# Kernel optimization log

Measured on AMD Instinct MI355X. Metric: run time of the kernel, lower is better.

## Reference

```python
import jax, jax.numpy as jnp
import numpy as np

NUM_EMBEDDINGS = 8192
EMBEDDING_DIM = 512
COMMITMENT_COST = 0.25
DECAY = 0.99
EPSILON = 1e-05


def setup_inputs() -> dict:
    key = jax.random.key(0)
    k1, k2, k3, k4 = jax.random.split(key, 4)
    z = jax.random.normal(k1, (16, 2048, EMBEDDING_DIM), dtype=jnp.float32)
    weight = jax.random.normal(k2, (NUM_EMBEDDINGS, EMBEDDING_DIM), dtype=jnp.float32)
    ema_cluster_size = jax.random.uniform(k3, (NUM_EMBEDDINGS,), dtype=jnp.float32)
    ema_w = jax.random.normal(k4, (NUM_EMBEDDINGS, EMBEDDING_DIM), dtype=jnp.float32)
    return {"z": z, "weight": weight, "ema_cluster_size": ema_cluster_size, "ema_w": ema_w}


def reference(z, weight, ema_cluster_size, ema_w):
    K, D = weight.shape
    z_flat = z.reshape(-1, D)                                   # [N, D]
    # squared-distance matrix via expanded GEMM (same math as torch)
    dist = ((z_flat ** 2).sum(1, keepdims=True)
            + (weight ** 2).sum(1)
            - 2.0 * z_flat @ weight.T)                          # [N, K]
    codes = jnp.argmin(dist, axis=1)                            # [N]
    # training-mode EMA update: one-hot sums expressed as segment_sum
    counts = jax.ops.segment_sum(jnp.ones(z_flat.shape[0], dtype=z.dtype), codes, num_segments=K)
    dw = jax.ops.segment_sum(z_flat, codes, num_segments=K)     # encodings.T @ z_flat
    new_cs = ema_cluster_size * DECAY + (1.0 - DECAY) * counts
    new_ema_w = ema_w * DECAY + (1.0 - DECAY) * dw
    n = new_cs.sum()
    cluster_size = (new_cs + EPSILON) / (n + K * EPSILON) * n
    new_weight = new_ema_w / cluster_size[:, None]              # updated codebook
    z_q = new_weight[codes].reshape(z.shape)                    # lookup with UPDATED weights
    vq_loss = COMMITMENT_COST * jnp.mean((jax.lax.stop_gradient(z_q) - z) ** 2)
    z_q_out = z + jax.lax.stop_gradient(z_q - z)                # straight-through estimator
    codes_out = codes.reshape(z.shape[0], -1)
    return vq_loss, z_q_out, codes_out, new_weight, new_cs, new_ema_w
```

## Files before the change

kernel.cpp:

```cpp
#include <hip/hip_runtime.h>
#include <cstdint>

#define K_CODES 8192
#define D_DIM   512
#define N_VEC   32768
#define DECAY   0.99f
#define EPS_VQ  1e-5f
#define COMMIT  0.25f
#define MARGIN  0.25f

typedef _Float16 half_t;
typedef _Float16 half8 __attribute__((ext_vector_type(8)));
typedef _Float16 half4 __attribute__((ext_vector_type(4)));
typedef float    f32x4 __attribute__((ext_vector_type(4)));
typedef unsigned long long u64;

#define GL2L(g, l)                                                              \
    __builtin_amdgcn_global_load_lds(                                           \
        (const __attribute__((address_space(1))) unsigned int*)(g),             \
        (__attribute__((address_space(3))) unsigned int*)(l), 16, 0, 0)

__device__ __forceinline__ unsigned ordf(float f) {
    unsigned u = __float_as_uint(f);
    return (u & 0x80000000u) ? ~u : (u | 0x80000000u);
}
__device__ __forceinline__ float unordf(unsigned u) {
    u = (u & 0x80000000u) ? (u & 0x7FFFFFFFu) : ~u;
    return __uint_as_float(u);
}


__global__ __launch_bounds__(256)
void conv_half_kernel(const float* __restrict__ x, half_t* __restrict__ out) {
    int i = blockIdx.x * 256 + threadIdx.x;
    float4 v = ((const float4*)x)[i];
    half4 h = { (_Float16)v.x, (_Float16)v.y, (_Float16)v.z, (_Float16)v.w };
    *(half4*)(out + (size_t)i * 4) = h;
}

__global__ __launch_bounds__(256)
void wsq_kernel(const float* __restrict__ w, float* __restrict__ wsq) {
    int wave = threadIdx.x >> 6, lane = threadIdx.x & 63;
    int row  = blockIdx.x * 4 + wave;
    const float4* p = (const float4*)(w + (size_t)row * D_DIM);
    float4 a = p[lane], b = p[lane + 64];
    float s = a.x*a.x + a.y*a.y + a.z*a.z + a.w*a.w
            + b.x*b.x + b.y*b.y + b.z*b.z + b.w*b.w;
    #pragma unroll
    for (int off = 32; off; off >>= 1) s += __shfl_down(s, off);
    if (lane == 0) wsq[row] = s;
}

__global__ __launch_bounds__(512, 2)
void dist1_kernel(const half_t* __restrict__ A, const half_t* __restrict__ B,
                  const float* __restrict__ wsq, uint4* __restrict__ partial) {
    __shared__ __align__(16) char smem[131072];
    half_t* A0 = (half_t*)smem;
    half_t* B0 = (half_t*)(smem + 32768);
    half_t* A1 = (half_t*)(smem + 65536);
    half_t* B1 = (half_t*)(smem + 98304);

    const int wg  = blockIdx.x;
    const int swz = (wg & 7) * 512 + (wg >> 3);
    const int k0  = (swz & 31) * 256;
    const int n0  = (swz >> 5) * 256;

    const int t    = threadIdx.x;
    const int lane = t & 63;
    const int wave = t >> 6;
    const int wm   = (wave >> 2) * 128;
    const int wn   = (wave & 3) * 64;
    const int l15  = lane & 15;
    const int q    = lane >> 4;

    const half_t* ga[4]; const half_t* gb[4];
    #pragma unroll
    for (int i = 0; i < 4; ++i) {
        int idx  = t + 512 * i;
        int row  = idx >> 3;
        int col8 = (idx & 7) ^ (row & 7);
        ga[i] = A + (size_t)(n0 + row) * D_DIM + col8 * 8;
        gb[i] = B + (size_t)(k0 + row) * D_DIM + col8 * 8;
    }

    f32x4 acc[8][4];
    #pragma unroll
    for (int mi = 0; mi < 8; ++mi)
        #pragma unroll
        for (int ni = 0; ni < 4; ++ni) acc[mi][ni] = (f32x4)0.0f;

    auto stage = [&](int kt, half_t* la, half_t* lb) {
        #pragma unroll
        for (int i = 0; i < 4; ++i) {
            GL2L(ga[i] + kt * 64, la + (size_t)(t + 512 * i) * 8);
            GL2L(gb[i] + kt * 64, lb + (size_t)(t + 512 * i) * 8);
        }
    };
    auto compute = [&](const half_t* la, const half_t* lb) {
        #pragma unroll
        for (int kk = 0; kk < 2; ++kk) {
            half8 af[8], bf[4];
            const int cpos = ((kk * 4 + q) ^ (l15 & 7)) * 8;
            #pragma unroll
            for (int mi = 0; mi < 8; ++mi)
                af[mi] = *(const half8*)&la[(wm + mi * 16 + l15) * 64 + cpos];
            #pragma unroll
            for (int ni = 0; ni < 4; ++ni)
                bf[ni] = *(const half8*)&lb[(wn + ni * 16 + l15) * 64 + cpos];
            __builtin_amdgcn_s_setprio(1);
            #pragma unroll
            for (int mi = 0; mi < 8; ++mi)
                #pragma unroll
                for (int ni = 0; ni < 4; ++ni)
                    acc[mi][ni] = __builtin_amdgcn_mfma_f32_16x16x32_f16(
                        af[mi], bf[ni], acc[mi][ni], 0, 0, 0);
            __builtin_amdgcn_s_setprio(0);
        }
    };

    stage(0, A0, B0);
    #pragma unroll
    for (int kt = 0; kt < 8; ++kt) {
        half_t* la = (kt & 1) ? A1 : A0;
        half_t* lb = (kt & 1) ? B1 : B0;
        if (kt < 7) {
            stage(kt + 1, (kt & 1) ? A0 : A1, (kt & 1) ? B0 : B1);
            asm volatile("s_waitcnt vmcnt(8)" ::: "memory");
        } else {
            asm volatile("s_waitcnt vmcnt(0)" ::: "memory");
        }
        __builtin_amdgcn_s_barrier();
        compute(la, lb);
        __builtin_amdgcn_s_barrier();
    }

    uint2* kp  = (uint2*)(smem + wave * 8704);
    uint2* fmp = (uint2*)(smem + 69632);

    float wb[4]; unsigned cb[4];
    #pragma unroll
    for (int ni = 0; ni < 4; ++ni) {
        wb[ni] = 512.0f - 0.5f * wsq[k0 + wn + ni * 16 + l15];
        cb[ni] = (unsigned)(wn + ni * 16 + l15);
    }

    uint2 res[2];
    #pragma unroll
    for (int half = 0; half < 2; ++half) {
        #pragma unroll
        for (int mi2 = 0; mi2 < 4; ++mi2) {
            const int mi = half * 4 + mi2;
            #pragma unroll
            for (int r = 0; r < 4; ++r) {
                unsigned k1 = 0u, k2 = 0u;
                #pragma unroll
                for (int ni = 0; ni < 4; ++ni) {
                    float a = acc[mi][ni][r] + wb[ni];
                    unsigned key = (__float_as_uint(a) & 0xFFFFFF00u) | cb[ni];
                    unsigned lo = min(k1, key);
                    k1 = max(k1, key);
                    k2 = max(k2, lo);
                }
                int row = mi2 * 16 + q * 4 + r;
                kp[row * 17 + l15] = make_uint2(k1, k2);
            }
        }
        const int rb = lane * 17;
        uint2 e0 = kp[rb];
        unsigned W1 = e0.x, W2 = e0.y;
        #pragma unroll
        for (int j = 1; j < 16; ++j) {
            uint2 e = kp[rb + j];
            unsigned lo = min(W1, e.x);
            W1 = max(W1, e.x);
            W2 = max(max(W2, lo), e.y);
        }
        res[half] = make_uint2(W1, W2);
    }
    fmp[(wm + lane) * 4 + (wave & 3)]      = res[0];
    fmp[(wm + 64 + lane) * 4 + (wave & 3)] = res[1];
    asm volatile("s_waitcnt lgkmcnt(0)" ::: "memory");
    __builtin_amdgcn_s_barrier();

    if (t < 256) {
        uint2 a = fmp[t * 4 + 0], b = fmp[t * 4 + 1];
        uint2 c = fmp[t * 4 + 2], d = fmp[t * 4 + 3];
        unsigned mab = max(a.x, b.x), mcd = max(c.x, d.x);
        unsigned sab = min(a.x, b.x), scd = min(c.x, d.x);
        unsigned W1 = max(mab, mcd);
        unsigned sec1 = max(min(mab, mcd), max(sab, scd));
        unsigned W2 = max(max(max(a.y, b.y), max(c.y, d.y)), sec1);
        unsigned col = (unsigned)k0 + (W1 & 255u);
        float v1 = __uint_as_float(W1 & 0xFFFFFF00u);
        float v2 = __uint_as_float(W2 & 0xFFFFFF00u);
        float d1 = 1024.0f - 2.0f * v1;
        float d2 = 1024.0f - 2.0f * v2;
        partial[(size_t)(swz & 31) * N_VEC + n0 + t] =
            make_uint4(col, ordf(d1), ordf(d2), 0u);
    }
}

__global__ __launch_bounds__(256)
void reduce_top2_kernel(const uint4* __restrict__ partial,
                        int* __restrict__ codes_i, float* __restrict__ codes_f,
                        int* __restrict__ cnt, int* __restrict__ list) {
    int row = blockIdx.x * 256 + threadIdx.x;
    u64 k1 = ~0ull, k2 = ~0ull;
    unsigned vm2 = 0xFFFFFFFFu;
    for (int kb = 0; kb < 32; ++kb) {
        uint4 e = partial[(size_t)kb * N_VEC + row];
        u64 k = ((u64)e.y << 32) | e.x;
        if (k < k1) { k2 = k1; k1 = k; }
        else if (k < k2) k2 = k;
        vm2 = min(vm2, e.z);
    }
    unsigned so = min((unsigned)(k2 >> 32), vm2);
    float bv = unordf((unsigned)(k1 >> 32));
    float sv = unordf(so);
    int code = (int)(k1 & 0xFFFFFFFFu);
    codes_i[row] = code;
    codes_f[row] = (float)code;
    if (sv - bv < MARGIN) { int p = atomicAdd(cnt, 1); list[p] = row; }
}

__global__ __launch_bounds__(256)
void refine2_kernel(const float* __restrict__ z, const float* __restrict__ w,
                    const float* __restrict__ wsq,
                    const int* __restrict__ cnt, const int* __restrict__ list,
                    u64* __restrict__ exact) {
    __shared__ float zs[64][68];
    __shared__ float ws[64][68];
    __shared__ int rows_s[64];
    const int n  = *cnt;
    const int c0 = blockIdx.x * 64;
    const int t  = threadIdx.x;
    const int lr = t & 63, lc = t >> 6;
    const int ty = t >> 4, tx = t & 15;

    for (int row0 = blockIdx.y * 64; row0 < n; row0 += gridDim.y * 64) {
        if (t < 64) {
            int ri = row0 + t;
            rows_s[t] = list[ri < n ? ri : n - 1];
        }
        __syncthreads();
        float acc[4][4] = {};
        const int zrow = rows_s[lr];
        for (int k0 = 0; k0 < D_DIM; k0 += 64) {
            #pragma unroll
            for (int it = 0; it < 4; ++it) {
                int kc = (lc * 4 + it) * 4;
                float4 v = *(const float4*)(z + (size_t)zrow * D_DIM + k0 + kc);
                zs[kc+0][lr] = v.x; zs[kc+1][lr] = v.y;
                zs[kc+2][lr] = v.z; zs[kc+3][lr] = v.w;
                float4 u = *(const float4*)(w + (size_t)(c0 + lr) * D_DIM + k0 + kc);
                ws[kc+0][lr] = u.x; ws[kc+1][lr] = u.y;
                ws[kc+2][lr] = u.z; ws[kc+3][lr] = u.w;
            }
            __syncthreads();
            #pragma unroll 8
            for (int k = 0; k < 64; ++k) {
                float4 za = *(const float4*)&zs[k][ty * 4];
                float4 wa = *(const float4*)&ws[k][tx * 4];
                float zav[4] = {za.x, za.y, za.z, za.w};
                float wav[4] = {wa.x, wa.y, wa.z, wa.w};
                #pragma unroll
                for (int i = 0; i < 4; ++i)
                    #pragma unroll
                    for (int j = 0; j < 4; ++j)
                        acc[i][j] += zav[i] * wav[j];
            }
            __syncthreads();
        }
        #pragma unroll
        for (int i = 0; i < 4; ++i) {
            u64 key = ~0ull;
            #pragma unroll
            for (int j = 0; j < 4; ++j) {
                int c = c0 + tx * 4 + j;
                float d = wsq[c] - 2.0f * acc[i][j];
                u64 k = ((u64)ordf(d) << 32) | (unsigned)c;
                if (k < key) key = k;
            }
            #pragma unroll
            for (int m = 1; m <= 8; m <<= 1) {
                u64 o = __shfl_xor(key, m);
                key = o < key ? o : key;
            }
            if (tx == 0) atomicMin(exact + rows_s[ty * 4 + i], key);
        }
        __syncthreads();
    }
}

__global__ __launch_bounds__(256)
void refine_fix_kernel(const int* __restrict__ cnt, const int* __restrict__ list,
                       const u64* __restrict__ exact,
                       int* __restrict__ codes_i, float* __restrict__ codes_f) {
    int n = *cnt;
    for (int i = blockIdx.x * 256 + threadIdx.x; i < n; i += 64 * 256) {
        int row = list[i];
        int code = (int)(exact[row] & 0xFFFFFFFFu);
        codes_i[row] = code;
        codes_f[row] = (float)code;
    }
}

__global__ __launch_bounds__(256)
void scatter_kernel(const int* __restrict__ codes_i, const float* __restrict__ z,
                    float* __restrict__ cnt_acc, float* __restrict__ dw_acc) {
    int row = blockIdx.x * 8 + (threadIdx.x >> 5);
    int c   = threadIdx.x & 31;
    int code = codes_i[row];
    if (c == 0) atomicAdd(&cnt_acc[code], 1.0f);
    const float* zr = z + (size_t)row * D_DIM;
    float* dr = dw_acc + (size_t)code * D_DIM;
    #pragma unroll
    for (int d = c; d < D_DIM; d += 32) atomicAdd(&dr[d], zr[d]);
}

__global__ __launch_bounds__(256)
void cs_kernel(const float* __restrict__ ema_cs, float* __restrict__ cs_out,
               float* __restrict__ nsum) {
    __shared__ float wsum[4];
    int i = blockIdx.x * 256 + threadIdx.x;
    float v = ema_cs[i] * DECAY + (1.0f - DECAY) * cs_out[i];
    cs_out[i] = v;
    float s = v;
    #pragma unroll
    for (int off = 32; off; off >>= 1) s += __shfl_down(s, off);
    int lane = threadIdx.x & 63, wid = threadIdx.x >> 6;
    if (lane == 0) wsum[wid] = s;
    __syncthreads();
    if (threadIdx.x == 0)
        atomicAdd(nsum, wsum[0] + wsum[1] + wsum[2] + wsum[3]);
}

__global__ __launch_bounds__(256)
void weight_kernel(const float* __restrict__ ema_w, const float* __restrict__ cs,
                   const float* __restrict__ nsum_p,
                   float* __restrict__ emaw_out, float* __restrict__ w_out) {
    int i = blockIdx.x * 256 + threadIdx.x;
    float dw = emaw_out[i];
    float ne = ema_w[i] * DECAY + (1.0f - DECAY) * dw;
    emaw_out[i] = ne;
    int k = i >> 9;
    float n = *nsum_p;
    float csize = (cs[k] + EPS_VQ) / (n + (float)K_CODES * EPS_VQ) * n;
    w_out[i] = ne / csize;
}

__global__ __launch_bounds__(256)
void gather_loss_kernel(const float* __restrict__ z, const int* __restrict__ codes,
                        const float* __restrict__ w, float* __restrict__ zq,
                        float* __restrict__ loss_acc) {
    __shared__ float wsum[4];
    int row  = blockIdx.x * 4 + (threadIdx.x >> 6);
    int lane = threadIdx.x & 63;
    int code = codes[row];
    const float* zr = z + (size_t)row * D_DIM;
    const float* wr = w + (size_t)code * D_DIM;
    float s = 0.0f;
    #pragma unroll
    for (int d = lane; d < D_DIM; d += 64) {
        float qv = wr[d];
        float diff = qv - zr[d];
        s += diff * diff;
        zq[(size_t)row * D_DIM + d] = qv;
    }
    #pragma unroll
    for (int off = 32; off; off >>= 1) s += __shfl_down(s, off);
    int wid = threadIdx.x >> 6;
    if (lane == 0) wsum[wid] = s;
    __syncthreads();
    if (threadIdx.x == 0)
        atomicAdd(loss_acc, wsum[0] + wsum[1] + wsum[2] + wsum[3]);
}

__global__ void finalize_kernel(const float* __restrict__ loss_acc,
                                float* __restrict__ out0) {
    *out0 = COMMIT * (*loss_acc) / 16777216.0f;
}

extern "C" void kernel_launch(void* const* d_in, const int* in_sizes, int n_in,
                              void* d_out, int out_size, void* d_ws, size_t ws_size,
                              hipStream_t stream) {
    const float* z      = (const float*)d_in[0];
    const float* weight = (const float*)d_in[1];
    const float* ema_cs = (const float*)d_in[2];
    const float* ema_w  = (const float*)d_in[3];

    float* out       = (float*)d_out;
    float* out_loss  = out;
    float* out_zq    = out + 1;
    float* out_codes = out + 16777217;
    float* out_w     = out + 16809985;
    float* out_cs    = out + 21004289;
    float* out_emaw  = out + 21012481;

    half_t* A_hi = (half_t*)(out + 4);
    half_t* B_hi = (half_t*)(out + 8388612);
    uint4*  partial = (uint4*)(out + 16809988);

    char* ws = (char*)d_ws;
    float* wsq      = (float*)ws;
    int*   codes_i  = (int*)(ws + 32768);
    int*   cnt      = (int*)(ws + 163840);
    float* nsum     = (float*)(ws + 163844);
    float* loss_acc = (float*)(ws + 163848);
    int*   list     = (int*)(ws + 163856);
    u64*   exact    = (u64*)(ws + 294928);

    hipMemsetAsync(cnt, 0, 16, stream);
    hipMemsetAsync(exact, 0xFF, N_VEC * 8, stream);

    conv_half_kernel<<<N_VEC * D_DIM / 1024, 256, 0, stream>>>(z, A_hi);
    conv_half_kernel<<<K_CODES * D_DIM / 1024, 256, 0, stream>>>(weight, B_hi);
    wsq_kernel<<<K_CODES / 4, 256, 0, stream>>>(weight, wsq);

    dist1_kernel<<<4096, 512, 0, stream>>>(A_hi, B_hi, wsq, partial);

    reduce_top2_kernel<<<N_VEC / 256, 256, 0, stream>>>(partial, codes_i,
                                                        out_codes, cnt, list);

    hipMemsetAsync(out_cs, 0, 8192 * 4, stream);
    hipMemsetAsync(out_emaw, 0, (size_t)4194304 * 4, stream);

    dim3 gr(K_CODES / 64, 64);
    refine2_kernel<<<gr, 256, 0, stream>>>(z, weight, wsq, cnt, list, exact);
    refine_fix_kernel<<<64, 256, 0, stream>>>(cnt, list, exact,
                                              codes_i, out_codes);

    scatter_kernel<<<N_VEC / 8, 256, 0, stream>>>(codes_i, z, out_cs, out_emaw);
    cs_kernel<<<K_CODES / 256, 256, 0, stream>>>(ema_cs, out_cs, nsum);
    weight_kernel<<<4194304 / 256, 256, 0, stream>>>(ema_w, out_cs, nsum,
                                                     out_emaw, out_w);
    gather_loss_kernel<<<N_VEC / 4, 256, 0, stream>>>(z, codes_i, out_w,
                                                      out_zq, loss_acc);
    finalize_kernel<<<1, 1, 0, stream>>>(loss_acc, out_loss);
}
```

Before: 918.7 us.

## Split GEMM K-tiles into half-stages with interleaved loads and fuse weight prep

The distance GEMM main loop now splits each 64-wide K tile into two 32-wide halves with a new LDS layout and XOR swizzle. Global-to-LDS staging of the next tile is interleaved between four MFMA sub-phases, with finer-grained vmcnt waits and more barriers. The goal is better overlap of memory traffic with MFMA work and smaller live fragment register sets. Separately, the weight fp16 conversion is fused into the squared-norm kernel to remove one launch and one read pass over the weights, at the cost of more barrier synchronisation inside the main loop.

```diff
diff --git a/kernel.cpp b/kernel.cpp
--- a/kernel.cpp
+++ b/kernel.cpp
@@ -39,11 +39,16 @@
 }
 
 __global__ __launch_bounds__(256)
-void wsq_kernel(const float* __restrict__ w, float* __restrict__ wsq) {
+void prep_w_kernel(const float* __restrict__ w, half_t* __restrict__ wh,
+                   float* __restrict__ wsq) {
     int wave = threadIdx.x >> 6, lane = threadIdx.x & 63;
     int row  = blockIdx.x * 4 + wave;
     const float4* p = (const float4*)(w + (size_t)row * D_DIM);
     float4 a = p[lane], b = p[lane + 64];
+    half4 ha = { (_Float16)a.x, (_Float16)a.y, (_Float16)a.z, (_Float16)a.w };
+    half4 hb = { (_Float16)b.x, (_Float16)b.y, (_Float16)b.z, (_Float16)b.w };
+    *(half4*)(wh + (size_t)row * D_DIM + lane * 4)       = ha;
+    *(half4*)(wh + (size_t)row * D_DIM + 256 + lane * 4) = hb;
     float s = a.x*a.x + a.y*a.y + a.z*a.z + a.w*a.w
             + b.x*b.x + b.y*b.y + b.z*b.z + b.w*b.w;
     #pragma unroll
@@ -55,10 +60,6 @@
 void dist1_kernel(const half_t* __restrict__ A, const half_t* __restrict__ B,
                   const float* __restrict__ wsq, uint4* __restrict__ partial) {
     __shared__ __align__(16) char smem[131072];
-    half_t* A0 = (half_t*)smem;
-    half_t* B0 = (half_t*)(smem + 32768);
-    half_t* A1 = (half_t*)(smem + 65536);
-    half_t* B1 = (half_t*)(smem + 98304);
 
     const int wg  = blockIdx.x;
     const int swz = (wg & 7) * 512 + (wg >> 3);
@@ -72,16 +73,92 @@
     const int wn   = (wave & 3) * 64;
     const int l15  = lane & 15;
     const int q    = lane >> 4;
-
-    const half_t* ga[4]; const half_t* gb[4];
-    #pragma unroll
-    for (int i = 0; i < 4; ++i) {
-        int idx  = t + 512 * i;
-        int row  = idx >> 3;
-        int col8 = (idx & 7) ^ (row & 7);
-        ga[i] = A + (size_t)(n0 + row) * D_DIM + col8 * 8;
-        gb[i] = B + (size_t)(k0 + row) * D_DIM + col8 * 8;
-    }
+    const int pos  = q ^ ((l15 >> 1) & 3);
+
+    const half_t* gsrcA[2]; const half_t* gsrcB[2]; int dsto[2];
+    #pragma unroll
+    for (int i = 0; i < 2; ++i) {
+        int idx = t + 512 * i;
+        int row = idx >> 2;
+        int cg  = (idx & 3) ^ ((row >> 1) & 3);
+        gsrcA[i] = A + (size_t)(n0 + row) * D_DIM + cg * 8;
+        gsrcB[i] = B + (size_t)(k0 + row) * D_DIM + cg * 8;
+        dsto[i]  = idx * 8;
+    }
+
+#define STAGE(isB, kh, Pdst, ktgt) do {                                      \
+    half_t* _d = (half_t*)(smem + ((Pdst) * 65536) +                         \
+                           ((isB) * 32768) + ((kh) * 16384));                \
+    GL2L(((isB) ? gsrcB[0] : gsrcA[0]) + (ktgt) * 64 + (kh) * 32,            \
+         _d + dsto[0]);                                                      \
+    GL2L(((isB) ? gsrcB[1] : gsrcA[1]) + (ktgt) * 64 + (kh) * 32,            \
+         _d + dsto[1]);                                                      \
+  } while (0)
+
+    const int afb = (wm + l15) * 32 + pos * 8;
+    const int bfb = (wn + l15) * 32 + pos * 8;
+
+#define LDAF(P, kh, mih) do {                                                \
+    const half_t* _s = (const half_t*)(smem + (P) * 65536 + (kh) * 16384);   \
+    af[0] = *(const half8*)&_s[afb + ((mih) * 4 + 0) * 512];                 \
+    af[1] = *(const half8*)&_s[afb + ((mih) * 4 + 1) * 512];                 \
+    af[2] = *(const half8*)&_s[afb + ((mih) * 4 + 2) * 512];                 \
+    af[3] = *(const half8*)&_s[afb + ((mih) * 4 + 3) * 512];                 \
+  } while (0)
+
+#define LDBF(P, kh) do {                                                     \
+    const half_t* _s = (const half_t*)(smem + (P) * 65536 + 32768 +          \
+                                       (kh) * 16384);                        \
+    bf[0] = *(const half8*)&_s[bfb + 0 * 512];                               \
+    bf[1] = *(const half8*)&_s[bfb + 1 * 512];                               \
+    bf[2] = *(const half8*)&_s[bfb + 2 * 512];                               \
+    bf[3] = *(const half8*)&_s[bfb + 3 * 512];                               \
+  } while (0)
+
+#define MFMA16(mih) do {                                                     \
+    __builtin_amdgcn_s_setprio(1);                                           \
+    _Pragma("unroll")                                                        \
+    for (int _j = 0; _j < 4; ++_j)                                           \
+        _Pragma("unroll")                                                    \
+        for (int _n = 0; _n < 4; ++_n)                                       \
+            acc[(mih) * 4 + _j][_n] = __builtin_amdgcn_mfma_f32_16x16x32_f16(\
+                af[_j], bf[_n], acc[(mih) * 4 + _j][_n], 0, 0, 0);           \
+    __builtin_amdgcn_s_setprio(0);                                           \
+  } while (0)
+
+#define BAR()  __builtin_amdgcn_s_barrier()
+#define VMC(N) asm volatile("s_waitcnt vmcnt(" #N ")" ::: "memory")
+
+#define TILE(P, ktgt, STG, LAST) do {                                        \
+    half8 af[4], bf[4];                                                      \
+                                \
+    LDAF(P, 0, 0); LDBF(P, 0);                                               \
+    if (STG) STAGE(0, 0, 1 - (P), ktgt);                                     \
+    BAR();                                                                   \
+    MFMA16(0);                                                               \
+    BAR();                                                                   \
+                                \
+    LDAF(P, 0, 1);                                                           \
+    if (STG) STAGE(1, 0, 1 - (P), ktgt);                                     \
+    BAR();                                                                   \
+    MFMA16(1);                                                               \
+    if (STG)       VMC(4);                                                   \
+    else if (LAST) VMC(0);                                                   \
+    BAR();                                                                   \
+                                \
+    LDAF(P, 1, 0); LDBF(P, 1);                                               \
+    if (STG) STAGE(0, 1, 1 - (P), ktgt);                                     \
+    BAR();                                                                   \
+    MFMA16(0);                                                               \
+    BAR();                                                                   \
+                                \
+    LDAF(P, 1, 1);                                                           \
+    if (STG) STAGE(1, 1, 1 - (P), ktgt);                                     \
+    BAR();                                                                   \
+    MFMA16(1);                                                               \
+    if (STG) VMC(4);                                                         \
+    BAR();                                                                   \
+  } while (0)
 
     f32x4 acc[8][4];
     #pragma unroll
@@ -89,50 +166,25 @@
         #pragma unroll
         for (int ni = 0; ni < 4; ++ni) acc[mi][ni] = (f32x4)0.0f;
 
-    auto stage = [&](int kt, half_t* la, half_t* lb) {
-        #pragma unroll
-        for (int i = 0; i < 4; ++i) {
-            GL2L(ga[i] + kt * 64, la + (size_t)(t + 512 * i) * 8);
-            GL2L(gb[i] + kt * 64, lb + (size_t)(t + 512 * i) * 8);
-        }
-    };
-    auto compute = [&](const half_t* la, const half_t* lb) {
-        #pragma unroll
-        for (int kk = 0; kk < 2; ++kk) {
-            half8 af[8], bf[4];
-            const int cpos = ((kk * 4 + q) ^ (l15 & 7)) * 8;
-            #pragma unroll
-            for (int mi = 0; mi < 8; ++mi)
-                af[mi] = *(const half8*)&la[(wm + mi * 16 + l15) * 64 + cpos];
-            #pragma unroll
-            for (int ni = 0; ni < 4; ++ni)
-                bf[ni] = *(const half8*)&lb[(wn + ni * 16 + l15) * 64 + cpos];
-            __builtin_amdgcn_s_setprio(1);
-            #pragma unroll
-            for (int mi = 0; mi < 8; ++mi)
-                #pragma unroll
-                for (int ni = 0; ni < 4; ++ni)
-                    acc[mi][ni] = __builtin_amdgcn_mfma_f32_16x16x32_f16(
-                        af[mi], bf[ni], acc[mi][ni], 0, 0, 0);
-            __builtin_amdgcn_s_setprio(0);
-        }
-    };
-
-    stage(0, A0, B0);
-    #pragma unroll
-    for (int kt = 0; kt < 8; ++kt) {
-        half_t* la = (kt & 1) ? A1 : A0;
-        half_t* lb = (kt & 1) ? B1 : B0;
-        if (kt < 7) {
-            stage(kt + 1, (kt & 1) ? A0 : A1, (kt & 1) ? B0 : B1);
-            asm volatile("s_waitcnt vmcnt(8)" ::: "memory");
-        } else {
-            asm volatile("s_waitcnt vmcnt(0)" ::: "memory");
-        }
-        __builtin_amdgcn_s_barrier();
-        compute(la, lb);
-        __builtin_amdgcn_s_barrier();
-    }
+    STAGE(0, 0, 0, 0); STAGE(1, 0, 0, 0); STAGE(0, 1, 0, 0); STAGE(1, 1, 0, 0);
+    VMC(4);
+    BAR();
+
+    #pragma unroll 1
+    for (int kt = 0; kt < 6; kt += 2) {
+        TILE(0, kt + 1, true, false);
+        TILE(1, kt + 2, true, false);
+    }
+    TILE(0, 7, true,  false);
+    TILE(1, 0, false, true);
+
+#undef STAGE
+#undef LDAF
+#undef LDBF
+#undef MFMA16
+#undef BAR
+#undef VMC
+#undef TILE
 
     uint2* kp  = (uint2*)(smem + wave * 8704);
     uint2* fmp = (uint2*)(smem + 69632);
@@ -179,8 +231,7 @@
     }
     fmp[(wm + lane) * 4 + (wave & 3)]      = res[0];
     fmp[(wm + 64 + lane) * 4 + (wave & 3)] = res[1];
-    asm volatile("s_waitcnt lgkmcnt(0)" ::: "memory");
-    __builtin_amdgcn_s_barrier();
+    __syncthreads();
 
     if (t < 256) {
         uint2 a = fmp[t * 4 + 0], b = fmp[t * 4 + 1];
@@ -414,8 +465,7 @@
     hipMemsetAsync(exact, 0xFF, N_VEC * 8, stream);
 
     conv_half_kernel<<<N_VEC * D_DIM / 1024, 256, 0, stream>>>(z, A_hi);
-    conv_half_kernel<<<K_CODES * D_DIM / 1024, 256, 0, stream>>>(weight, B_hi);
-    wsq_kernel<<<K_CODES / 4, 256, 0, stream>>>(weight, wsq);
+    prep_w_kernel<<<K_CODES / 4, 256, 0, stream>>>(weight, B_hi, wsq);
 
     dist1_kernel<<<4096, 512, 0, stream>>>(A_hi, B_hi, wsq, partial);
 
```

Result: no change. 908.4 us (-1.1%).
